# Kernel optimization log

Hardware: AMD Instinct MI355X
Metric: run time of the kernel (lower is better)

## Reference

```python
import jax, jax.numpy as jnp
import numpy as np

E = 8       # n_experts
K = 2       # k_experts
D_IN = 1024
D_OUT = 1024
D_EXP = 2048
N = 16384   # tokens (batch*seq, forward requires 2D input)


def setup_inputs() -> dict:
    key = jax.random.key(0)
    ks = jax.random.split(key, 4)
    x = jax.random.normal(ks[0], (N, D_IN), jnp.float32)
    Wg = jax.random.normal(ks[1], (E, D_IN), jnp.float32) * 0.02      # router weight
    bg = jnp.zeros((E,), jnp.float32)                                  # router bias
    W_in = jax.random.normal(ks[2], (E, D_EXP, D_IN), jnp.float32) * 0.02
    b_in = jnp.zeros((E, D_EXP), jnp.float32)                          # w_in_bias_init=0.0
    W_out = jax.random.normal(ks[3], (E, D_OUT, D_EXP), jnp.float32) * 0.02  # bias=False
    return {"x": x, "Wg": Wg, "bg": bg, "W_in": W_in, "b_in": b_in, "W_out": W_out}


def moe_forward(x, Wg, bg, W_in, b_in, W_out):
    # Eval mode: gate jitter / solu jitter / dropouts are training-only no-ops.
    n = x.shape[0]
    # --- routing ---
    logits = x @ Wg.T + bg                                 # [N, E]
    probs = jax.nn.softmax(logits, axis=-1)
    mean_probs = probs.mean(axis=0)                        # [E]
    k_vals, k_idx = jax.lax.top_k(probs, K)                # [N, K]
    k_w = k_vals / k_vals.sum(axis=-1, keepdims=True)      # renormalized gate weights
    counts = jnp.bincount(k_idx.reshape(-1), length=E)     # [E] int
    load_balancing_loss = E * jnp.sum((counts.astype(x.dtype) / n) * mean_probs)
    # --- dispatch + expert w_in (loop over fixed small E; combine with one-hot mask) ---
    sel = jax.nn.one_hot(k_idx, E, dtype=x.dtype)          # [N, K, E]
    h = jnp.zeros((n, K, D_EXP), x.dtype)                  # preacts per (token, slot)
    for e in range(E):
        he = x @ W_in[e].T + b_in[e]                       # [N, D_EXP]
        h = h + sel[:, :, e][..., None] * he[:, None, :]
    # --- SoLU (eval): softmax(preacts) * preacts over hidden dim ---
    acts = jax.nn.softmax(h, axis=-1) * h                  # [N, K, D_EXP]
    # --- expert w_out (no bias) ---
    out = jnp.zeros((n, K, D_OUT), x.dtype)
    for e in range(E):
        oe = jnp.einsum('nkh,oh->nko', acts, W_out[e])
        out = out + sel[:, :, e][..., None] * oe
    # --- weighted combine over the K chosen experts ---
    outputs = (out * k_w[..., None]).sum(axis=1)           # [N, D_OUT]
    return outputs, load_balancing_loss


def reference(x, Wg, bg, W_in, b_in, W_out):
    return moe_forward(x, Wg, bg, W_in, b_in, W_out)
```

## Files before the change

kernel.cpp:

```cpp
#include <hip/hip_runtime.h>
#include <hip/hip_bf16.h>
#include <stdint.h>

#define E_EXP 8
#define NTOK  16384
#define DIN   1024
#define DEXP  2048
#define DOUT  1024
#define NSLOT (NTOK*2)
#define MAXT  264

typedef __attribute__((ext_vector_type(8))) short short8;
typedef __attribute__((ext_vector_type(8))) unsigned short ushort8;
typedef __attribute__((ext_vector_type(4))) float f32x4;

__device__ __forceinline__ unsigned short f2bf(float f){
  union { float f; uint32_t u; } v; v.f = f;
  uint32_t r = (v.u + 0x7FFFu + ((v.u >> 16) & 1u)) >> 16;
  return (unsigned short)r;
}
__device__ __forceinline__ float bf2f(unsigned short u){
  union { uint32_t u; float f; } v; v.u = ((uint32_t)u) << 16;
  return v.f;
}

__device__ __forceinline__ void async16(const void* g, void* l){
  __builtin_amdgcn_global_load_lds(
      (const __attribute__((address_space(1))) void*)g,
      (__attribute__((address_space(3))) void*)l, 16, 0, 0);
}

__global__ __launch_bounds__(256) void cast_bf16(const float* __restrict__ s,
                                                 unsigned short* __restrict__ d, int n){
  int i = (blockIdx.x*256 + threadIdx.x)*8;
  if (i >= n) return;
  float4 a = *(const float4*)(s+i);
  float4 b = *(const float4*)(s+i+4);
  ushort8 o;
  o[0]=f2bf(a.x); o[1]=f2bf(a.y); o[2]=f2bf(a.z); o[3]=f2bf(a.w);
  o[4]=f2bf(b.x); o[5]=f2bf(b.y); o[6]=f2bf(b.z); o[7]=f2bf(b.w);
  *(ushort8*)(d+i) = o;
}

__global__ __launch_bounds__(256) void router(
    const float* __restrict__ x, const float* __restrict__ Wg, const float* __restrict__ bg,
    int* __restrict__ eidx, float* __restrict__ gw,
    int* __restrict__ counts, float* __restrict__ probsum)
{
  __shared__ float sWg[E_EXP*DIN];
  __shared__ float sps[E_EXP];
  __shared__ int   scnt[E_EXP];
  const int tid = threadIdx.x;
  for (int i = tid; i < E_EXP*DIN; i += 256) sWg[i] = Wg[i];
  if (tid < E_EXP){ sps[tid]=0.f; scnt[tid]=0; }
  __syncthreads();
  const int lane = tid & 63;
  const int wv   = tid >> 6;
  for (int it = 0; it < 16; ++it){
    const int token = blockIdx.x*64 + wv*16 + it;
    float4 xv[4];
#pragma unroll
    for (int j=0;j<4;++j) xv[j] = *(const float4*)&x[(size_t)token*DIN + j*256 + lane*4];
    float p[E_EXP];
#pragma unroll
    for (int e2=0;e2<E_EXP;++e2){
      float s = 0.f;
#pragma unroll
      for (int j=0;j<4;++j){
        const float4 w4 = *(const float4*)&sWg[e2*DIN + j*256 + lane*4];
        s += xv[j].x*w4.x + xv[j].y*w4.y + xv[j].z*w4.z + xv[j].w*w4.w;
      }
      p[e2] = s;
    }
#pragma unroll
    for (int d=1; d<64; d<<=1){
#pragma unroll
      for (int e2=0;e2<E_EXP;++e2) p[e2] += __shfl_xor(p[e2], d);
    }
    if (lane == 0){
      float mx = -1e30f;
#pragma unroll
      for (int e2=0;e2<E_EXP;++e2){ p[e2] += bg[e2]; mx = fmaxf(mx, p[e2]); }
      float se = 0.f;
#pragma unroll
      for (int e2=0;e2<E_EXP;++e2){ p[e2] = __expf(p[e2]-mx); se += p[e2]; }
      const float inv = 1.f/se;
#pragma unroll
      for (int e2=0;e2<E_EXP;++e2){ p[e2] *= inv; atomicAdd(&sps[e2], p[e2]); }
      int i1 = 0;
#pragma unroll
      for (int e2=1;e2<E_EXP;++e2) if (p[e2] > p[i1]) i1 = e2;
      int i2 = (i1==0) ? 1 : 0;
#pragma unroll
      for (int e2=0;e2<E_EXP;++e2) if (e2 != i1 && p[e2] > p[i2]) i2 = e2;
      const float v1 = p[i1], v2 = p[i2], s12 = v1 + v2;
      eidx[2*token]   = i1; eidx[2*token+1] = i2;
      gw[2*token]     = v1/s12; gw[2*token+1] = v2/s12;
      atomicAdd(&scnt[i1], 1); atomicAdd(&scnt[i2], 1);
    }
  }
  __syncthreads();
  if (tid < E_EXP){ atomicAdd(&counts[tid], scnt[tid]); atomicAdd(&probsum[tid], sps[tid]); }
}

__global__ void finalize(const int* __restrict__ counts, const float* __restrict__ probsum,
                         float* __restrict__ loss_out, int* __restrict__ offs,
                         int* __restrict__ cursor, int* __restrict__ tile_e,
                         int* __restrict__ tile_row, int* __restrict__ ntiles)
{
  if (threadIdx.x != 0 || blockIdx.x != 0) return;
  int off = 0, nt = 0;
  float loss = 0.f;
  offs[0] = 0;
  for (int e2=0;e2<E_EXP;++e2){
    const int c = counts[e2];
    loss += (float)c * probsum[e2];
    cursor[e2] = 0;
    const int t = (c + 127) >> 7;
    for (int i=0;i<t;++i){ tile_e[nt] = e2; tile_row[nt] = off + i*128; ++nt; }
    off += c;
    offs[e2+1] = off;
  }
  *ntiles = nt;
  *loss_out = loss * (8.f/((float)NTOK*(float)NTOK));
}

__global__ __launch_bounds__(256) void scatter(const int* __restrict__ eidx, const float* __restrict__ gw,
    const int* __restrict__ offs, int* __restrict__ cursor,
    int* __restrict__ ptok, float* __restrict__ pw)
{
  const int t = blockIdx.x*256 + threadIdx.x;
  if (t >= NTOK) return;
#pragma unroll
  for (int s=0;s<2;++s){
    const int e2  = eidx[2*t+s];
    const int pos = offs[e2] + atomicAdd(&cursor[e2], 1);
    ptok[pos] = t;
    pw[pos]   = gw[2*t+s];
  }
}

__global__ __launch_bounds__(256) void gemm1(
    const unsigned short* __restrict__ xb,
    const unsigned short* __restrict__ wib,
    const float* __restrict__ b_in,
    unsigned short* __restrict__ H,
    const int* __restrict__ ptok,
    const int* __restrict__ offs,
    const int* __restrict__ tile_e,
    const int* __restrict__ tile_row,
    const int* __restrict__ ntiles)
{
  if ((int)blockIdx.x >= *ntiles) return;
  const int e    = tile_e[blockIdx.x];
  const int row0 = tile_row[blockIdx.x];
  const int seg_end = offs[e+1];
  const int col0 = blockIdx.y * 128;

  __shared__ unsigned short As[128*64];
  __shared__ unsigned short Bs[128*64];

  const int tid  = threadIdx.x;
  const int lane = tid & 63;
  const int wv   = tid >> 6;
  const int wm   = wv >> 1, wn = wv & 1;
  const int crow = lane >> 3;
  const int ck   = (lane & 7) * 8;

  const unsigned short* ag[4];
  const unsigned short* bg4[4];
  unsigned short* al[4];
  unsigned short* bl[4];
#pragma unroll
  for (int i = 0; i < 4; ++i){
    const int chunk = wv*4 + i;
    const int row = chunk*8 + crow;
    int g = row0 + row; if (g > NSLOT-1) g = NSLOT-1;
    const int tok = ptok[g];
    ag[i]  = xb + (size_t)tok*DIN + ck;
    bg4[i] = wib + ((size_t)e*DEXP + col0 + row)*DIN + ck;
    al[i]  = &As[chunk*512];
    bl[i]  = &Bs[chunk*512];
  }

  f32x4 acc[4][4] = {};

  for (int kt = 0; kt < DIN; kt += 64){
#pragma unroll
    for (int i = 0; i < 4; ++i){
      async16(ag[i] + kt, al[i]);
      async16(bg4[i] + kt, bl[i]);
    }
    __syncthreads();
#pragma unroll
    for (int kk = 0; kk < 2; ++kk){
      const int krd = kk*32 + (lane>>4)*8;
      short8 a[4], b[4];
#pragma unroll
      for (int m = 0; m < 4; ++m)
        a[m] = *(const short8*)&As[(wm*64 + m*16 + (lane&15))*64 + krd];
#pragma unroll
      for (int n = 0; n < 4; ++n)
        b[n] = *(const short8*)&Bs[(wn*64 + n*16 + (lane&15))*64 + krd];
#pragma unroll
      for (int m = 0; m < 4; ++m)
#pragma unroll
        for (int n = 0; n < 4; ++n)
          acc[m][n] = __builtin_amdgcn_mfma_f32_16x16x32_bf16(a[m], b[n], acc[m][n], 0, 0, 0);
    }
    __syncthreads();
  }

  float bias[4];
#pragma unroll
  for (int n = 0; n < 4; ++n)
    bias[n] = b_in[e*DEXP + col0 + wn*64 + n*16 + (lane&15)];

#pragma unroll
  for (int m = 0; m < 4; ++m){
#pragma unroll
    for (int j = 0; j < 4; ++j){
      const int r = wm*64 + m*16 + (lane>>4)*4 + j;
      const int g = row0 + r;
      if (g < seg_end){
#pragma unroll
        for (int n = 0; n < 4; ++n){
          const int c = col0 + wn*64 + n*16 + (lane&15);
          H[(size_t)g*DEXP + c] = f2bf(acc[m][n][j] + bias[n]);
        }
      }
    }
  }
}

__global__ __launch_bounds__(256) void solu(unsigned short* __restrict__ H){
  const size_t row = blockIdx.x;
  unsigned short* hp = H + row*DEXP;
  const int tid  = threadIdx.x;
  const int lane = tid & 63;
  const int wv   = tid >> 6;
  const short8 hv = *(const short8*)&hp[tid*8];
  float f[8];
#pragma unroll
  for (int j=0;j<8;++j) f[j] = bf2f((unsigned short)hv[j]);
  float mx = f[0];
#pragma unroll
  for (int j=1;j<8;++j) mx = fmaxf(mx, f[j]);
  for (int d=1; d<64; d<<=1) mx = fmaxf(mx, __shfl_xor(mx, d));
  __shared__ float redm[4];
  __shared__ float reds[4];
  if (lane==0) redm[wv] = mx;
  __syncthreads();
  mx = fmaxf(fmaxf(redm[0],redm[1]), fmaxf(redm[2],redm[3]));
  float se = 0.f; float ex[8];
#pragma unroll
  for (int j=0;j<8;++j){ ex[j] = __expf(f[j]-mx); se += ex[j]; }
  for (int d=1; d<64; d<<=1) se += __shfl_xor(se, d);
  if (lane==0) reds[wv] = se;
  __syncthreads();
  se = reds[0]+reds[1]+reds[2]+reds[3];
  const float inv = 1.0f/se;
  ushort8 o;
#pragma unroll
  for (int j=0;j<8;++j) o[j] = f2bf(f[j]*ex[j]*inv);
  *(ushort8*)&hp[tid*8] = o;
}

__global__ __launch_bounds__(256) void gemm2(
    const unsigned short* __restrict__ ACT,
    const unsigned short* __restrict__ wob,
    float* __restrict__ out,
    const int* __restrict__ ptok,
    const float* __restrict__ pw,
    const int* __restrict__ offs,
    const int* __restrict__ tile_e,
    const int* __restrict__ tile_row,
    const int* __restrict__ ntiles)
{
  if ((int)blockIdx.x >= *ntiles) return;
  const int e    = tile_e[blockIdx.x];
  const int row0 = tile_row[blockIdx.x];
  const int seg_end = offs[e+1];
  const int col0 = blockIdx.y * 128;

  __shared__ unsigned short As[128*64];
  __shared__ unsigned short Bs[128*64];

  const int tid  = threadIdx.x;
  const int lane = tid & 63;
  const int wv   = tid >> 6;
  const int wm   = wv >> 1, wn = wv & 1;
  const int crow = lane >> 3;
  const int ck   = (lane & 7) * 8;

  const unsigned short* ag[4];
  const unsigned short* bg4[4];
  unsigned short* al[4];
  unsigned short* bl[4];
#pragma unroll
  for (int i = 0; i < 4; ++i){
    const int chunk = wv*4 + i;
    const int row = chunk*8 + crow;
    int g = row0 + row; if (g > NSLOT-1) g = NSLOT-1;
    ag[i]  = ACT + (size_t)g*DEXP + ck;
    bg4[i] = wob + ((size_t)e*DOUT + col0 + row)*DEXP + ck;
    al[i]  = &As[chunk*512];
    bl[i]  = &Bs[chunk*512];
  }

  f32x4 acc[4][4] = {};

  for (int kt = 0; kt < DEXP; kt += 64){
#pragma unroll
    for (int i = 0; i < 4; ++i){
      async16(ag[i] + kt, al[i]);
      async16(bg4[i] + kt, bl[i]);
    }
    __syncthreads();
#pragma unroll
    for (int kk = 0; kk < 2; ++kk){
      const int krd = kk*32 + (lane>>4)*8;
      short8 a[4], b[4];
#pragma unroll
      for (int m = 0; m < 4; ++m)
        a[m] = *(const short8*)&As[(wm*64 + m*16 + (lane&15))*64 + krd];
#pragma unroll
      for (int n = 0; n < 4; ++n)
        b[n] = *(const short8*)&Bs[(wn*64 + n*16 + (lane&15))*64 + krd];
#pragma unroll
      for (int m = 0; m < 4; ++m)
#pragma unroll
        for (int n = 0; n < 4; ++n)
          acc[m][n] = __builtin_amdgcn_mfma_f32_16x16x32_bf16(a[m], b[n], acc[m][n], 0, 0, 0);
    }
    __syncthreads();
  }

#pragma unroll
  for (int m = 0; m < 4; ++m){
#pragma unroll
    for (int j = 0; j < 4; ++j){
      const int r = wm*64 + m*16 + (lane>>4)*4 + j;
      const int g = row0 + r;
      if (g < seg_end){
        const int tok   = ptok[g];
        const float wgt = pw[g];
        float* op = out + (size_t)tok*DOUT;
#pragma unroll
        for (int n = 0; n < 4; ++n){
          const int c = col0 + wn*64 + n*16 + (lane&15);
          unsafeAtomicAdd(op + c, wgt * acc[m][n][j]);
        }
      }
    }
  }
}

extern "C" void kernel_launch(void* const* d_in, const int* in_sizes, int n_in,
                              void* d_out, int out_size, void* d_ws, size_t ws_size,
                              hipStream_t stream)
{
  const float* x     = (const float*)d_in[0];
  const float* Wg    = (const float*)d_in[1];
  const float* bgp   = (const float*)d_in[2];
  const float* W_in  = (const float*)d_in[3];
  const float* b_in  = (const float*)d_in[4];
  const float* W_out = (const float*)d_in[5];
  float* out = (float*)d_out;

  char* base = (char*)d_ws;
  size_t o = 0;
  unsigned short* xb  = (unsigned short*)(base + o); o += (size_t)NTOK*DIN*2;
  unsigned short* wib = (unsigned short*)(base + o); o += (size_t)E_EXP*DEXP*DIN*2;
  unsigned short* wob = (unsigned short*)(base + o); o += (size_t)E_EXP*DOUT*DEXP*2;
  unsigned short* H   = (unsigned short*)(base + o); o += (size_t)NSLOT*DEXP*2;
  int*   eidx    = (int*)(base + o);   o += (size_t)NSLOT*4;
  float* gw      = (float*)(base + o); o += (size_t)NSLOT*4;
  int*   ptok    = (int*)(base + o);   o += (size_t)NSLOT*4;
  float* pw      = (float*)(base + o); o += (size_t)NSLOT*4;
  int*   counts  = (int*)(base + o);   o += 32;
  float* probsum = (float*)(base + o); o += 32;
  int*   cursor  = (int*)(base + o);   o += 32;
  int*   offs    = (int*)(base + o);   o += 64;
  int*   tile_e  = (int*)(base + o);   o += (size_t)MAXT*4;
  int*   tile_row= (int*)(base + o);   o += (size_t)MAXT*4;
  int*   ntiles  = (int*)(base + o);   o += 64;

  hipMemsetAsync(d_out, 0, (size_t)(NTOK*(size_t)DOUT + 1)*4, stream);
  hipMemsetAsync(counts, 0, 96, stream);

  cast_bf16<<<dim3(8192), 256, 0, stream>>>(x,     xb,  NTOK*DIN);
  cast_bf16<<<dim3(8192), 256, 0, stream>>>(W_in,  wib, E_EXP*DEXP*DIN);
  cast_bf16<<<dim3(8192), 256, 0, stream>>>(W_out, wob, E_EXP*DOUT*DEXP);

  router<<<dim3(256), 256, 0, stream>>>(x, Wg, bgp, eidx, gw, counts, probsum);
  finalize<<<dim3(1), 64, 0, stream>>>(counts, probsum, out + (size_t)NTOK*DOUT,
                                       offs, cursor, tile_e, tile_row, ntiles);
  scatter<<<dim3(64), 256, 0, stream>>>(eidx, gw, offs, cursor, ptok, pw);

  gemm1<<<dim3(MAXT, DEXP/128), 256, 0, stream>>>(xb, wib, b_in, H, ptok, offs,
                                                  tile_e, tile_row, ntiles);
  solu<<<dim3(NSLOT), 256, 0, stream>>>(H);
  gemm2<<<dim3(MAXT, DOUT/128), 256, 0, stream>>>(H, wob, out, ptok, pw, offs,
                                                  tile_e, tile_row, ntiles);
}
```

Measured before the change: 916.8 us.

## Double-buffer LDS tiles with XOR swizzle in expert GEMMs

Both expert GEMM kernels now keep two LDS stages, issuing the async global-to-LDS loads for the next k-tile before computing the current one, with manual vmcnt waits and raw barriers. This is meant to hide global-load latency behind the MFMA work. The LDS layout is also XOR-swizzled on the 16-byte chunk index to reduce bank conflicts on the short8 reads, and s_setprio raises wave priority during the MFMA section. Doubling LDS per block to 64KB may lower occupancy, and the hand-written wait counts depend on the exact number of outstanding loads.

```diff
diff --git a/kernel.cpp b/kernel.cpp
--- a/kernel.cpp
+++ b/kernel.cpp
@@ -29,6 +29,10 @@
       (const __attribute__((address_space(1))) void*)g,
       (__attribute__((address_space(3))) void*)l, 16, 0, 0);
 }
+
+#define VMCNT8() asm volatile("s_waitcnt vmcnt(8)" ::: "memory")
+#define VMCNT0() asm volatile("s_waitcnt vmcnt(0)" ::: "memory")
+#define BARRIER() do { asm volatile("" ::: "memory"); __builtin_amdgcn_s_barrier(); asm volatile("" ::: "memory"); } while(0)
 
 __global__ __launch_bounds__(256) void cast_bf16(const float* __restrict__ s,
                                                  unsigned short* __restrict__ d, int n){
@@ -157,58 +161,76 @@
   const int seg_end = offs[e+1];
   const int col0 = blockIdx.y * 128;
 
-  __shared__ unsigned short As[128*64];
-  __shared__ unsigned short Bs[128*64];
+  __shared__ unsigned short As[2][128*64];
+  __shared__ unsigned short Bs[2][128*64];
 
   const int tid  = threadIdx.x;
   const int lane = tid & 63;
   const int wv   = tid >> 6;
   const int wm   = wv >> 1, wn = wv & 1;
   const int crow = lane >> 3;
-  const int ck   = (lane & 7) * 8;
+  const int cks  = ((lane & 7) ^ crow) * 8;
 
   const unsigned short* ag[4];
   const unsigned short* bg4[4];
-  unsigned short* al[4];
-  unsigned short* bl[4];
+  unsigned int alo[4], blo[4];
 #pragma unroll
   for (int i = 0; i < 4; ++i){
     const int chunk = wv*4 + i;
     const int row = chunk*8 + crow;
     int g = row0 + row; if (g > NSLOT-1) g = NSLOT-1;
     const int tok = ptok[g];
-    ag[i]  = xb + (size_t)tok*DIN + ck;
-    bg4[i] = wib + ((size_t)e*DEXP + col0 + row)*DIN + ck;
-    al[i]  = &As[chunk*512];
-    bl[i]  = &Bs[chunk*512];
+    ag[i]  = xb + (size_t)tok*DIN + cks;
+    bg4[i] = wib + ((size_t)e*DEXP + col0 + row)*DIN + cks;
+    alo[i] = chunk*512;
+    blo[i] = chunk*512;
   }
 
   f32x4 acc[4][4] = {};
-
-  for (int kt = 0; kt < DIN; kt += 64){
-#pragma unroll
-    for (int i = 0; i < 4; ++i){
-      async16(ag[i] + kt, al[i]);
-      async16(bg4[i] + kt, bl[i]);
-    }
-    __syncthreads();
+  const int NK = DIN/64;
+  int cur = 0;
+
+#pragma unroll
+  for (int i = 0; i < 4; ++i){
+    async16(ag[i],  &As[0][alo[i]]);
+    async16(bg4[i], &Bs[0][blo[i]]);
+  }
+
+#pragma unroll 2
+  for (int kt = 0; kt < NK; ++kt){
+    BARRIER();
+    if (kt + 1 < NK){
+      const int ko = (kt+1)*64;
+#pragma unroll
+      for (int i = 0; i < 4; ++i){
+        async16(ag[i]  + ko, &As[cur^1][alo[i]]);
+        async16(bg4[i] + ko, &Bs[cur^1][blo[i]]);
+      }
+      VMCNT8();
+    } else {
+      VMCNT0();
+    }
+    BARRIER();
+
+    __builtin_amdgcn_s_setprio(1);
 #pragma unroll
     for (int kk = 0; kk < 2; ++kk){
-      const int krd = kk*32 + (lane>>4)*8;
+      const int ksl = ((kk*4 + (lane>>4)) ^ (lane & 7)) * 8;
       short8 a[4], b[4];
 #pragma unroll
       for (int m = 0; m < 4; ++m)
-        a[m] = *(const short8*)&As[(wm*64 + m*16 + (lane&15))*64 + krd];
+        a[m] = *(const short8*)&As[cur][(wm*64 + m*16 + (lane&15))*64 + ksl];
 #pragma unroll
       for (int n = 0; n < 4; ++n)
-        b[n] = *(const short8*)&Bs[(wn*64 + n*16 + (lane&15))*64 + krd];
+        b[n] = *(const short8*)&Bs[cur][(wn*64 + n*16 + (lane&15))*64 + ksl];
 #pragma unroll
       for (int m = 0; m < 4; ++m)
 #pragma unroll
         for (int n = 0; n < 4; ++n)
           acc[m][n] = __builtin_amdgcn_mfma_f32_16x16x32_bf16(a[m], b[n], acc[m][n], 0, 0, 0);
     }
-    __syncthreads();
+    __builtin_amdgcn_s_setprio(0);
+    cur ^= 1;
   }
 
   float bias[4];
@@ -283,57 +305,75 @@
   const int seg_end = offs[e+1];
   const int col0 = blockIdx.y * 128;
 
-  __shared__ unsigned short As[128*64];
-  __shared__ unsigned short Bs[128*64];
+  __shared__ unsigned short As[2][128*64];
+  __shared__ unsigned short Bs[2][128*64];
 
   const int tid  = threadIdx.x;
   const int lane = tid & 63;
   const int wv   = tid >> 6;
   const int wm   = wv >> 1, wn = wv & 1;
   const int crow = lane >> 3;
-  const int ck   = (lane & 7) * 8;
+  const int cks  = ((lane & 7) ^ crow) * 8;
 
   const unsigned short* ag[4];
   const unsigned short* bg4[4];
-  unsigned short* al[4];
-  unsigned short* bl[4];
+  unsigned int alo[4], blo[4];
 #pragma unroll
   for (int i = 0; i < 4; ++i){
     const int chunk = wv*4 + i;
     const int row = chunk*8 + crow;
     int g = row0 + row; if (g > NSLOT-1) g = NSLOT-1;
-    ag[i]  = ACT + (size_t)g*DEXP + ck;
-    bg4[i] = wob + ((size_t)e*DOUT + col0 + row)*DEXP + ck;
-    al[i]  = &As[chunk*512];
-    bl[i]  = &Bs[chunk*512];
+    ag[i]  = ACT + (size_t)g*DEXP + cks;
+    bg4[i] = wob + ((size_t)e*DOUT + col0 + row)*DEXP + cks;
+    alo[i] = chunk*512;
+    blo[i] = chunk*512;
   }
 
   f32x4 acc[4][4] = {};
-
-  for (int kt = 0; kt < DEXP; kt += 64){
-#pragma unroll
-    for (int i = 0; i < 4; ++i){
-      async16(ag[i] + kt, al[i]);
-      async16(bg4[i] + kt, bl[i]);
-    }
-    __syncthreads();
+  const int NK = DEXP/64;
+  int cur = 0;
+
+#pragma unroll
+  for (int i = 0; i < 4; ++i){
+    async16(ag[i],  &As[0][alo[i]]);
+    async16(bg4[i], &Bs[0][blo[i]]);
+  }
+
+#pragma unroll 2
+  for (int kt = 0; kt < NK; ++kt){
+    BARRIER();
+    if (kt + 1 < NK){
+      const int ko = (kt+1)*64;
+#pragma unroll
+      for (int i = 0; i < 4; ++i){
+        async16(ag[i]  + ko, &As[cur^1][alo[i]]);
+        async16(bg4[i] + ko, &Bs[cur^1][blo[i]]);
+      }
+      VMCNT8();
+    } else {
+      VMCNT0();
+    }
+    BARRIER();
+
+    __builtin_amdgcn_s_setprio(1);
 #pragma unroll
     for (int kk = 0; kk < 2; ++kk){
-      const int krd = kk*32 + (lane>>4)*8;
+      const int ksl = ((kk*4 + (lane>>4)) ^ (lane & 7)) * 8;
       short8 a[4], b[4];
 #pragma unroll
       for (int m = 0; m < 4; ++m)
-        a[m] = *(const short8*)&As[(wm*64 + m*16 + (lane&15))*64 + krd];
+        a[m] = *(const short8*)&As[cur][(wm*64 + m*16 + (lane&15))*64 + ksl];
 #pragma unroll
       for (int n = 0; n < 4; ++n)
-        b[n] = *(const short8*)&Bs[(wn*64 + n*16 + (lane&15))*64 + krd];
+        b[n] = *(const short8*)&Bs[cur][(wn*64 + n*16 + (lane&15))*64 + ksl];
 #pragma unroll
       for (int m = 0; m < 4; ++m)
 #pragma unroll
         for (int n = 0; n < 4; ++n)
           acc[m][n] = __builtin_amdgcn_mfma_f32_16x16x32_bf16(a[m], b[n], acc[m][n], 0, 0, 0);
     }
-    __syncthreads();
+    __builtin_amdgcn_s_setprio(0);
+    cur ^= 1;
   }
 
 #pragma unroll
```

New measurement: 871.3 us. 1.05x faster.

## Swizzle LDS tiles, swap grid axes, fuse x bf16 cast into router

Applied to the files above, without the earlier changes.

The GEMM kernels now XOR-swizzle the 16-byte chunk index when loading into LDS and when reading it back, to avoid bank conflicts on the MFMA operand reads. The grid is transposed so column tiles vary fastest, meaning consecutive blocks share the same token rows and expert weights, which should improve L2 reuse. The x-to-bf16 cast is folded into the router, which already reads x, removing one kernel launch and one full pass over x. The swizzle must match between the global-to-LDS and LDS read addressing, and the fused cast adds stores to the router.

```diff
diff --git a/kernel.cpp b/kernel.cpp
--- a/kernel.cpp
+++ b/kernel.cpp
@@ -12,6 +12,7 @@
 
 typedef __attribute__((ext_vector_type(8))) short short8;
 typedef __attribute__((ext_vector_type(8))) unsigned short ushort8;
+typedef __attribute__((ext_vector_type(4))) unsigned short ushort4v;
 typedef __attribute__((ext_vector_type(4))) float f32x4;
 
 __device__ __forceinline__ unsigned short f2bf(float f){
@@ -44,6 +45,7 @@
 
 __global__ __launch_bounds__(256) void router(
     const float* __restrict__ x, const float* __restrict__ Wg, const float* __restrict__ bg,
+    unsigned short* __restrict__ xb,
     int* __restrict__ eidx, float* __restrict__ gw,
     int* __restrict__ counts, float* __restrict__ probsum)
 {
@@ -61,6 +63,12 @@
     float4 xv[4];
 #pragma unroll
     for (int j=0;j<4;++j) xv[j] = *(const float4*)&x[(size_t)token*DIN + j*256 + lane*4];
+#pragma unroll
+    for (int j=0;j<4;++j){
+      ushort4v o;
+      o[0]=f2bf(xv[j].x); o[1]=f2bf(xv[j].y); o[2]=f2bf(xv[j].z); o[3]=f2bf(xv[j].w);
+      *(ushort4v*)&xb[(size_t)token*DIN + j*256 + lane*4] = o;
+    }
     float p[E_EXP];
 #pragma unroll
     for (int e2=0;e2<E_EXP;++e2){
@@ -151,11 +159,11 @@
     const int* __restrict__ tile_row,
     const int* __restrict__ ntiles)
 {
-  if ((int)blockIdx.x >= *ntiles) return;
-  const int e    = tile_e[blockIdx.x];
-  const int row0 = tile_row[blockIdx.x];
+  if ((int)blockIdx.y >= *ntiles) return;
+  const int e    = tile_e[blockIdx.y];
+  const int row0 = tile_row[blockIdx.y];
   const int seg_end = offs[e+1];
-  const int col0 = blockIdx.y * 128;
+  const int col0 = blockIdx.x * 128;
 
   __shared__ unsigned short As[128*64];
   __shared__ unsigned short Bs[128*64];
@@ -165,22 +173,20 @@
   const int wv   = tid >> 6;
   const int wm   = wv >> 1, wn = wv & 1;
   const int crow = lane >> 3;
-  const int ck   = (lane & 7) * 8;
+  const int cks  = ((lane & 7) ^ crow) * 8;
 
   const unsigned short* ag[4];
   const unsigned short* bg4[4];
-  unsigned short* al[4];
-  unsigned short* bl[4];
+  unsigned int alo[4];
 #pragma unroll
   for (int i = 0; i < 4; ++i){
     const int chunk = wv*4 + i;
     const int row = chunk*8 + crow;
     int g = row0 + row; if (g > NSLOT-1) g = NSLOT-1;
     const int tok = ptok[g];
-    ag[i]  = xb + (size_t)tok*DIN + ck;
-    bg4[i] = wib + ((size_t)e*DEXP + col0 + row)*DIN + ck;
-    al[i]  = &As[chunk*512];
-    bl[i]  = &Bs[chunk*512];
+    ag[i]  = xb + (size_t)tok*DIN + cks;
+    bg4[i] = wib + ((size_t)e*DEXP + col0 + row)*DIN + cks;
+    alo[i] = chunk*512;
   }
 
   f32x4 acc[4][4] = {};
@@ -188,20 +194,20 @@
   for (int kt = 0; kt < DIN; kt += 64){
 #pragma unroll
     for (int i = 0; i < 4; ++i){
-      async16(ag[i] + kt, al[i]);
-      async16(bg4[i] + kt, bl[i]);
+      async16(ag[i]  + kt, &As[alo[i]]);
+      async16(bg4[i] + kt, &Bs[alo[i]]);
     }
     __syncthreads();
 #pragma unroll
     for (int kk = 0; kk < 2; ++kk){
-      const int krd = kk*32 + (lane>>4)*8;
+      const int ksl = ((kk*4 + (lane>>4)) ^ (lane & 7)) * 8;
       short8 a[4], b[4];
 #pragma unroll
       for (int m = 0; m < 4; ++m)
-        a[m] = *(const short8*)&As[(wm*64 + m*16 + (lane&15))*64 + krd];
+        a[m] = *(const short8*)&As[(wm*64 + m*16 + (lane&15))*64 + ksl];
 #pragma unroll
       for (int n = 0; n < 4; ++n)
-        b[n] = *(const short8*)&Bs[(wn*64 + n*16 + (lane&15))*64 + krd];
+        b[n] = *(const short8*)&Bs[(wn*64 + n*16 + (lane&15))*64 + ksl];
 #pragma unroll
       for (int m = 0; m < 4; ++m)
 #pragma unroll
@@ -277,11 +283,11 @@
     const int* __restrict__ tile_row,
     const int* __restrict__ ntiles)
 {
-  if ((int)blockIdx.x >= *ntiles) return;
-  const int e    = tile_e[blockIdx.x];
-  const int row0 = tile_row[blockIdx.x];
+  if ((int)blockIdx.y >= *ntiles) return;
+  const int e    = tile_e[blockIdx.y];
+  const int row0 = tile_row[blockIdx.y];
   const int seg_end = offs[e+1];
-  const int col0 = blockIdx.y * 128;
+  const int col0 = blockIdx.x * 128;
 
   __shared__ unsigned short As[128*64];
   __shared__ unsigned short Bs[128*64];
@@ -291,21 +297,19 @@
   const int wv   = tid >> 6;
   const int wm   = wv >> 1, wn = wv & 1;
   const int crow = lane >> 3;
-  const int ck   = (lane & 7) * 8;
+  const int cks  = ((lane & 7) ^ crow) * 8;
 
   const unsigned short* ag[4];
   const unsigned short* bg4[4];
-  unsigned short* al[4];
-  unsigned short* bl[4];
+  unsigned int alo[4];
 #pragma unroll
   for (int i = 0; i < 4; ++i){
     const int chunk = wv*4 + i;
     const int row = chunk*8 + crow;
     int g = row0 + row; if (g > NSLOT-1) g = NSLOT-1;
-    ag[i]  = ACT + (size_t)g*DEXP + ck;
-    bg4[i] = wob + ((size_t)e*DOUT + col0 + row)*DEXP + ck;
-    al[i]  = &As[chunk*512];
-    bl[i]  = &Bs[chunk*512];
+    ag[i]  = ACT + (size_t)g*DEXP + cks;
+    bg4[i] = wob + ((size_t)e*DOUT + col0 + row)*DEXP + cks;
+    alo[i] = chunk*512;
   }
 
   f32x4 acc[4][4] = {};
@@ -313,20 +317,20 @@
   for (int kt = 0; kt < DEXP; kt += 64){
 #pragma unroll
     for (int i = 0; i < 4; ++i){
-      async16(ag[i] + kt, al[i]);
-      async16(bg4[i] + kt, bl[i]);
+      async16(ag[i]  + kt, &As[alo[i]]);
+      async16(bg4[i] + kt, &Bs[alo[i]]);
     }
     __syncthreads();
 #pragma unroll
     for (int kk = 0; kk < 2; ++kk){
-      const int krd = kk*32 + (lane>>4)*8;
+      const int ksl = ((kk*4 + (lane>>4)) ^ (lane & 7)) * 8;
       short8 a[4], b[4];
 #pragma unroll
       for (int m = 0; m < 4; ++m)
-        a[m] = *(const short8*)&As[(wm*64 + m*16 + (lane&15))*64 + krd];
+        a[m] = *(const short8*)&As[(wm*64 + m*16 + (lane&15))*64 + ksl];
 #pragma unroll
       for (int n = 0; n < 4; ++n)
-        b[n] = *(const short8*)&Bs[(wn*64 + n*16 + (lane&15))*64 + krd];
+        b[n] = *(const short8*)&Bs[(wn*64 + n*16 + (lane&15))*64 + ksl];
 #pragma unroll
       for (int m = 0; m < 4; ++m)
 #pragma unroll
@@ -389,18 +393,17 @@
   hipMemsetAsync(d_out, 0, (size_t)(NTOK*(size_t)DOUT + 1)*4, stream);
   hipMemsetAsync(counts, 0, 96, stream);
 
-  cast_bf16<<<dim3(8192), 256, 0, stream>>>(x,     xb,  NTOK*DIN);
   cast_bf16<<<dim3(8192), 256, 0, stream>>>(W_in,  wib, E_EXP*DEXP*DIN);
   cast_bf16<<<dim3(8192), 256, 0, stream>>>(W_out, wob, E_EXP*DOUT*DEXP);
 
-  router<<<dim3(256), 256, 0, stream>>>(x, Wg, bgp, eidx, gw, counts, probsum);
+  router<<<dim3(256), 256, 0, stream>>>(x, Wg, bgp, xb, eidx, gw, counts, probsum);
   finalize<<<dim3(1), 64, 0, stream>>>(counts, probsum, out + (size_t)NTOK*DOUT,
                                        offs, cursor, tile_e, tile_row, ntiles);
   scatter<<<dim3(64), 256, 0, stream>>>(eidx, gw, offs, cursor, ptok, pw);
 
-  gemm1<<<dim3(MAXT, DEXP/128), 256, 0, stream>>>(xb, wib, b_in, H, ptok, offs,
+  gemm1<<<dim3(DEXP/128, MAXT), 256, 0, stream>>>(xb, wib, b_in, H, ptok, offs,
                                                   tile_e, tile_row, ntiles);
   solu<<<dim3(NSLOT), 256, 0, stream>>>(H);
-  gemm2<<<dim3(MAXT, DOUT/128), 256, 0, stream>>>(H, wob, out, ptok, pw, offs,
+  gemm2<<<dim3(DOUT/128, MAXT), 256, 0, stream>>>(H, wob, out, ptok, pw, offs,
                                                   tile_e, tile_row, ntiles);
 }
```

Result: faster. 858.6 us (-6.3%).
